# Optimization experiments

Hardware: AMD Instinct MI355X
Metric: run time of the kernel (lower is better)

The kernel has to match this reference:

```python
import jax, jax.numpy as jnp
import numpy as np

F = 128          # feature_size
C = 300          # n_content_dims
V = 100001       # n_nodes + 1 (embedding rows)
N0, N1, N2 = 409600, 40960, 4096   # NodeFlow layer sizes (fanout ~10)
E0, E1 = 409600, 40960             # edges in block0 (L0->L1) and block1 (L1->L2)


def setup_inputs() -> dict:
    key = jax.random.key(0)
    ks = jax.random.split(key, 24)
    std = 1.0 / F
    xav_p = float(np.sqrt(6.0 / (C + F)))   # xavier_uniform for proj Linear(C->F)
    xav_c = float(np.sqrt(6.0 / (2 * F + F)))  # xavier_uniform for conv Linear(2F->F)
    return {
        'nid0': jax.random.randint(ks[0], (N0,), 0, 100000),
        'nid1': jax.random.randint(ks[1], (N1,), 0, 100000),
        'nid2': jax.random.randint(ks[2], (N2,), 0, 100000),
        'content0': jax.random.normal(ks[3], (N0, C), jnp.float32),
        'content1': jax.random.normal(ks[4], (N1, C), jnp.float32),
        'content2': jax.random.normal(ks[5], (N2, C), jnp.float32),
        'block0_src': jax.random.randint(ks[6], (E0,), 0, N0),
        'block0_dst': jax.random.randint(ks[7], (E0,), 0, N1),
        'block1_src': jax.random.randint(ks[8], (E1,), 0, N1),
        'block1_dst': jax.random.randint(ks[9], (E1,), 0, N2),
        'node_emb': jax.random.normal(ks[10], (V, F), jnp.float32) * std,
        'Wp0': jax.random.uniform(ks[11], (F, C), jnp.float32, -xav_p, xav_p),
        'bp0': jnp.zeros((F,), jnp.float32),
        'Wp1': jax.random.uniform(ks[12], (F, C), jnp.float32, -xav_p, xav_p),
        'bp1': jnp.zeros((F,), jnp.float32),
        'Wp2': jax.random.uniform(ks[13], (F, C), jnp.float32, -xav_p, xav_p),
        'bp2': jnp.zeros((F,), jnp.float32),
        'Wc0': jax.random.uniform(ks[14], (F, 2 * F), jnp.float32, -xav_c, xav_c),
        'bc0': jnp.zeros((F,), jnp.float32),
        'Wc1': jax.random.uniform(ks[15], (F, 2 * F), jnp.float32, -xav_c, xav_c),
        'bc1': jnp.zeros((F,), jnp.float32),
    }


def _embed(node_emb, nid, content, Wp, bp):
    # h = node_emb(nid + 1) + LeakyReLU(content @ Wp.T + bp)   (dropout is eval no-op)
    return node_emb[nid + 1] + jax.nn.leaky_relu(content @ Wp.T + bp)


def _conv(h_src, src, dst, h_self, n_dst, W, b):
    # DGL block_compute: copy_src('h')+sum -> h_agg ; copy_src('one')+sum -> w
    msgs = h_src[src]                                    # [E, F] gather
    h_agg = jax.ops.segment_sum(msgs, dst, num_segments=n_dst)
    w = jax.ops.segment_sum(jnp.ones((src.shape[0],), h_src.dtype), dst,
                            num_segments=n_dst)
    h_agg = (h_agg - h_self) / jnp.maximum(w - 1.0, 1.0)[:, None]
    h_new = jax.nn.leaky_relu(jnp.concatenate([h_self, h_agg], axis=1) @ W.T + b)
    nrm = jnp.maximum(jnp.linalg.norm(h_new, axis=1, keepdims=True), 1e-6)
    return h_new / nrm


def reference(nid0, nid1, nid2, content0, content1, content2,
              block0_src, block0_dst, block1_src, block1_dst,
              node_emb, Wp0, bp0, Wp1, bp1, Wp2, bp2,
              Wc0, bc0, Wc1, bc1):
    h0 = _embed(node_emb, nid0, content0, Wp0, bp0)   # [N0, F]
    h1 = _embed(node_emb, nid1, content1, Wp1, bp1)   # [N1, F]
    h2 = _embed(node_emb, nid2, content2, Wp2, bp2)   # [N2, F]
    h1 = _conv(h0, block0_src, block0_dst, h1, N1, Wc0, bc0)
    h2 = _conv(h1, block1_src, block1_dst, h2, N2, Wc1, bc1)
    return h2
```

## Files before the change

### kernel.cpp

```cpp
#include <hip/hip_runtime.h>
#include <hip/hip_bf16.h>
#include <math.h>

#define F 128
#define C 300
#define CKP 320
#define K2F 256
#define N0_ 409600
#define N1_ 40960
#define N2_ 4096
#define E0_ 409600
#define E1_ 40960
#define CAP 64
#define LDA 40

typedef unsigned short u16;
typedef unsigned int u32;
typedef __attribute__((ext_vector_type(8))) short short8;
typedef __attribute__((ext_vector_type(8))) unsigned short u16x8;
typedef __attribute__((ext_vector_type(4))) float f32x4;

__device__ __forceinline__ float lrelu(float x) { return x > 0.f ? x : 0.01f * x; }

__device__ __forceinline__ u16 f2bf(float x) {
  __hip_bfloat16 h = __float2bfloat16(x);
  u16 r; __builtin_memcpy(&r, &h, 2); return r;
}
__device__ __forceinline__ float bf2f(u16 v) {
  union { u32 u; float f; } c; c.u = ((u32)v) << 16; return c.f;
}

#define GLOAD_LDS16(gp, lp) \
  __builtin_amdgcn_global_load_lds( \
      (const __attribute__((address_space(1))) void*)(const void*)(gp), \
      (__attribute__((address_space(3))) void*)(lp), 16, 0, 0)

__global__ __launch_bounds__(256) void zero_kernel(float4* __restrict__ p, int n4) {
  int i = blockIdx.x * 256 + threadIdx.x;
  if (i < n4) p[i] = make_float4(0.f, 0.f, 0.f, 0.f);
}

__global__ __launch_bounds__(256) void convert_all(
    const float* __restrict__ Wp0, const float* __restrict__ Wp1,
    const float* __restrict__ Wp2, const float* __restrict__ Wc0,
    const float* __restrict__ Wc1,
    u16* __restrict__ Wpb0, u16* __restrict__ Wpb1, u16* __restrict__ Wpb2,
    u16* __restrict__ Wcb0, u16* __restrict__ Wcb1)
{
  int i = blockIdx.x * 256 + threadIdx.x;
  const int P = F * CKP, Q = F * K2F;
  const float* W; u16* O; int K, KP, j;
  if      (i < P)         { W = Wp0; O = Wpb0; K = C;   KP = CKP; j = i; }
  else if (i < 2 * P)     { W = Wp1; O = Wpb1; K = C;   KP = CKP; j = i - P; }
  else if (i < 3 * P)     { W = Wp2; O = Wpb2; K = C;   KP = CKP; j = i - 2 * P; }
  else if (i < 3 * P + Q) { W = Wc0; O = Wcb0; K = K2F; KP = K2F; j = i - 3 * P; }
  else if (i < 3 * P + 2 * Q) { W = Wc1; O = Wcb1; K = K2F; KP = K2F; j = i - 3 * P - Q; }
  else return;
  int f = j / KP, k = j - f * KP;
  O[j] = (k < K) ? f2bf(W[(size_t)f * K + k]) : (u16)0;
}

__global__ __launch_bounds__(256) void build_csr(
    const int* __restrict__ b0s, const int* __restrict__ b0d,
    const int* __restrict__ b1s, const int* __restrict__ b1d,
    int* __restrict__ deg0, int* __restrict__ deg1,
    int* __restrict__ csr0, int* __restrict__ csr1)
{
  int e = blockIdx.x * 256 + threadIdx.x;
  if (e < E0_) {
    int d = b0d[e];
    int slot = atomicAdd(&deg0[d], 1);
    if (slot < CAP) csr0[(size_t)d * CAP + slot] = b0s[e];
  } else {
    int e1 = e - E0_;
    if (e1 < E1_) {
      int d = b1d[e1];
      int slot = atomicAdd(&deg1[d], 1);
      if (slot < CAP) csr1[(size_t)d * CAP + slot] = b1s[e1];
    }
  }
}

__global__ __launch_bounds__(256) void embed_mfma(
    const float* __restrict__ content, const u16* __restrict__ Wpb,
    const float* __restrict__ bp, const int* __restrict__ nid,
    const float* __restrict__ emb, u16* __restrict__ out, int ostride,
    const float* __restrict__ zpad)
{
  __shared__ float As[2][128 * 32];
  __shared__ u16  Bs[2][128 * 32];
  const int t = threadIdx.x;
  const int lane = t & 63, w = t >> 6;
  const int row0 = blockIdx.x * 128;

  f32x4 acc[2][8];
#pragma unroll
  for (int fr = 0; fr < 2; ++fr)
#pragma unroll
    for (int fc = 0; fc < 8; ++fc) {
      acc[fr][fc][0] = 0.f; acc[fr][fc][1] = 0.f;
      acc[fr][fc][2] = 0.f; acc[fr][fc][3] = 0.f;
    }

  const int a_rl = lane >> 3, a_u = lane & 7;
  const int b_rl = lane >> 2, b_u = lane & 3;

  auto stage = [&](int buf, int k0) {
#pragma unroll
    for (int i = 0; i < 4; ++i) {
      int r = w * 32 + i * 8 + a_rl;
      int v = a_u ^ (r & 7);
      const float* gp = (k0 == 288 && v >= 3)
          ? (zpad + v * 4)
          : (content + (size_t)(row0 + r) * C + k0 + v * 4);
      GLOAD_LDS16(gp, &As[buf][(w * 32 + i * 8) * 32]);
    }
#pragma unroll
    for (int j = 0; j < 2; ++j) {
      int r = w * 32 + j * 16 + b_rl;
      int v = b_u ^ (r & 3);
      const u16* gp = Wpb + (size_t)r * CKP + k0 + v * 8;
      GLOAD_LDS16(gp, &Bs[buf][(w * 32 + j * 16) * 32]);
    }
  };

  stage(0, 0);
  __syncthreads();

  const int frow = lane & 15, g = lane >> 4;
  const int nt = CKP / 32;
  int cur = 0;
  for (int tstep = 0; tstep < nt; ++tstep) {
    if (tstep + 1 < nt) stage(cur ^ 1, (tstep + 1) * 32);

    const int sw = frow & 7;
    const int u0 = (2 * g) ^ sw, u1 = (2 * g + 1) ^ sw;
    int ra0 = (w * 32 + frow) * 32, ra1 = (w * 32 + 16 + frow) * 32;
    float4 fa00 = *(const float4*)&As[cur][ra0 + u0 * 4];
    float4 fa01 = *(const float4*)&As[cur][ra0 + u1 * 4];
    float4 fa10 = *(const float4*)&As[cur][ra1 + u0 * 4];
    float4 fa11 = *(const float4*)&As[cur][ra1 + u1 * 4];
    u16x8 a0v, a1v;
    a0v[0]=f2bf(fa00.x); a0v[1]=f2bf(fa00.y); a0v[2]=f2bf(fa00.z); a0v[3]=f2bf(fa00.w);
    a0v[4]=f2bf(fa01.x); a0v[5]=f2bf(fa01.y); a0v[6]=f2bf(fa01.z); a0v[7]=f2bf(fa01.w);
    a1v[0]=f2bf(fa10.x); a1v[1]=f2bf(fa10.y); a1v[2]=f2bf(fa10.z); a1v[3]=f2bf(fa10.w);
    a1v[4]=f2bf(fa11.x); a1v[5]=f2bf(fa11.y); a1v[6]=f2bf(fa11.z); a1v[7]=f2bf(fa11.w);
    short8 a0 = *(short8*)&a0v, a1 = *(short8*)&a1v;

    const int bswz = frow & 3;
#pragma unroll
    for (int fc = 0; fc < 8; ++fc) {
      int rb = (fc * 16 + frow) * 32 + (g ^ bswz) * 8;
      short8 b = *(const short8*)&Bs[cur][rb];
      acc[0][fc] = __builtin_amdgcn_mfma_f32_16x16x32_bf16(a0, b, acc[0][fc], 0, 0, 0);
      acc[1][fc] = __builtin_amdgcn_mfma_f32_16x16x32_bf16(a1, b, acc[1][fc], 0, 0, 0);
    }
    __syncthreads();
    cur ^= 1;
  }

  float bpv[8];
#pragma unroll
  for (int fc = 0; fc < 8; ++fc) bpv[fc] = bp[fc * 16 + frow];
#pragma unroll
  for (int fr = 0; fr < 2; ++fr) {
#pragma unroll
    for (int q = 0; q < 4; ++q) {
      int n = row0 + w * 32 + fr * 16 + g * 4 + q;
      int gi = nid[n] + 1;
      const float* erow = emb + (size_t)gi * F;
      u16* orow = out + (size_t)n * ostride;
#pragma unroll
      for (int fc = 0; fc < 8; ++fc) {
        int col = fc * 16 + frow;
        float v = acc[fr][fc][q] + bpv[fc];
        orow[col] = f2bf(erow[col] + lrelu(v));
      }
    }
  }
}

__global__ __launch_bounds__(256) void gather_xa(
    const u16* __restrict__ hsrc, const int* __restrict__ csr,
    const int* __restrict__ deg, u16* __restrict__ xcat)
{
  int d = blockIdx.x * 4 + (threadIdx.x >> 6);
  int lane = threadIdx.x & 63;
  u32 hv = *(const u32*)&xcat[(size_t)d * (2 * F) + lane * 2];
  float h0f = bf2f((u16)(hv & 0xffff)), h1f = bf2f((u16)(hv >> 16));
  int dg = deg[d];
  int n = dg < CAP ? dg : CAP;
  const int* cp = csr + (size_t)d * CAP;
  float s0 = 0.f, s1 = 0.f;
  int j = 0;
  for (; j + 4 <= n; j += 4) {
    int i0 = cp[j], i1 = cp[j + 1], i2 = cp[j + 2], i3 = cp[j + 3];
    u32 v0 = *(const u32*)&hsrc[(size_t)i0 * F + lane * 2];
    u32 v1 = *(const u32*)&hsrc[(size_t)i1 * F + lane * 2];
    u32 v2 = *(const u32*)&hsrc[(size_t)i2 * F + lane * 2];
    u32 v3 = *(const u32*)&hsrc[(size_t)i3 * F + lane * 2];
    s0 += bf2f((u16)(v0 & 0xffff)) + bf2f((u16)(v1 & 0xffff))
        + bf2f((u16)(v2 & 0xffff)) + bf2f((u16)(v3 & 0xffff));
    s1 += bf2f((u16)(v0 >> 16)) + bf2f((u16)(v1 >> 16))
        + bf2f((u16)(v2 >> 16)) + bf2f((u16)(v3 >> 16));
  }
  for (; j < n; ++j) {
    u32 v = *(const u32*)&hsrc[(size_t)cp[j] * F + lane * 2];
    s0 += bf2f((u16)(v & 0xffff));
    s1 += bf2f((u16)(v >> 16));
  }
  float inv = 1.f / fmaxf((float)dg - 1.f, 1.f);
  u16 a0 = f2bf((s0 - h0f) * inv), a1 = f2bf((s1 - h1f) * inv);
  *(u32*)&xcat[(size_t)d * (2 * F) + F + lane * 2] = ((u32)a1 << 16) | a0;
}

template<int F32OUT>
__global__ __launch_bounds__(256) void conv_mfma(
    const u16* __restrict__ xcat, const u16* __restrict__ Wcb,
    const float* __restrict__ bc, u16* __restrict__ outb,
    float* __restrict__ outf)
{
  __shared__ u16 As[128][LDA];
  __shared__ u16 Bs[128][LDA];
  const int t = threadIdx.x;
  const int lane = t & 63, w = t >> 6;
  const int row0 = blockIdx.x * 128;

  f32x4 acc[2][8];
#pragma unroll
  for (int fr = 0; fr < 2; ++fr)
#pragma unroll
    for (int fc = 0; fc < 8; ++fc) {
      acc[fr][fc][0] = 0.f; acc[fr][fc][1] = 0.f;
      acc[fr][fc][2] = 0.f; acc[fr][fc][3] = 0.f;
    }

  for (int k0 = 0; k0 < K2F; k0 += 32) {
    if (k0) __syncthreads();
#pragma unroll
    for (int it = 0; it < 2; ++it) {
      int cc = it * 256 + t;
      int r = cc >> 2, kc = (cc & 3) * 8;
      *(u16x8*)&As[r][kc] = *(const u16x8*)&xcat[(size_t)(row0 + r) * K2F + k0 + kc];
      *(u16x8*)&Bs[r][kc] = *(const u16x8*)&Wcb[(size_t)r * K2F + k0 + kc];
    }
    __syncthreads();

    const int frow = lane & 15;
    const int kc = (lane >> 4) * 8;
    short8 a0 = *(const short8*)&As[w * 32 + frow][kc];
    short8 a1 = *(const short8*)&As[w * 32 + 16 + frow][kc];
#pragma unroll
    for (int fc = 0; fc < 8; ++fc) {
      short8 b = *(const short8*)&Bs[fc * 16 + frow][kc];
      acc[0][fc] = __builtin_amdgcn_mfma_f32_16x16x32_bf16(a0, b, acc[0][fc], 0, 0, 0);
      acc[1][fc] = __builtin_amdgcn_mfma_f32_16x16x32_bf16(a1, b, acc[1][fc], 0, 0, 0);
    }
  }

  float bcv[8];
#pragma unroll
  for (int fc = 0; fc < 8; ++fc) bcv[fc] = bc[fc * 16 + (lane & 15)];
#pragma unroll
  for (int fr = 0; fr < 2; ++fr) {
#pragma unroll
    for (int q = 0; q < 4; ++q) {
      float x[8];
      float ss = 0.f;
#pragma unroll
      for (int fc = 0; fc < 8; ++fc) {
        x[fc] = lrelu(acc[fr][fc][q] + bcv[fc]);
        ss += x[fc] * x[fc];
      }
#pragma unroll
      for (int m = 8; m >= 1; m >>= 1) ss += __shfl_xor(ss, m, 64);
      float nrm = 1.f / fmaxf(sqrtf(ss), 1e-6f);
      int n = row0 + w * 32 + fr * 16 + (lane >> 4) * 4 + q;
#pragma unroll
      for (int fc = 0; fc < 8; ++fc) {
        int col = fc * 16 + (lane & 15);
        if (F32OUT) outf[(size_t)n * F + col] = x[fc] * nrm;
        else        outb[(size_t)n * F + col] = f2bf(x[fc] * nrm);
      }
    }
  }
}

extern "C" void kernel_launch(void* const* d_in, const int* in_sizes, int n_in,
                              void* d_out, int out_size, void* d_ws, size_t ws_size,
                              hipStream_t stream) {
  const int*   nid0     = (const int*)d_in[0];
  const int*   nid1     = (const int*)d_in[1];
  const int*   nid2     = (const int*)d_in[2];
  const float* content0 = (const float*)d_in[3];
  const float* content1 = (const float*)d_in[4];
  const float* content2 = (const float*)d_in[5];
  const int*   b0s      = (const int*)d_in[6];
  const int*   b0d      = (const int*)d_in[7];
  const int*   b1s      = (const int*)d_in[8];
  const int*   b1d      = (const int*)d_in[9];
  const float* emb      = (const float*)d_in[10];
  const float* Wp0      = (const float*)d_in[11];
  const float* bp0      = (const float*)d_in[12];
  const float* Wp1      = (const float*)d_in[13];
  const float* bp1      = (const float*)d_in[14];
  const float* Wp2      = (const float*)d_in[15];
  const float* bp2      = (const float*)d_in[16];
  const float* Wc0      = (const float*)d_in[17];
  const float* bc0      = (const float*)d_in[18];
  const float* Wc1      = (const float*)d_in[19];
  const float* bc1      = (const float*)d_in[20];

  u16* wsu = (u16*)d_ws;
  u16* h0b   = wsu;
  u16* xcat1 = h0b + (size_t)N0_ * F;
  u16* xcat2 = xcat1 + (size_t)N1_ * 2 * F;
  u16* h1nb  = xcat2 + (size_t)N2_ * 2 * F;
  u16* Wpb0  = h1nb + (size_t)N1_ * F;
  u16* Wpb1  = Wpb0 + (size_t)F * CKP;
  u16* Wpb2  = Wpb1 + (size_t)F * CKP;
  u16* Wcb0  = Wpb2 + (size_t)F * CKP;
  u16* Wcb1  = Wcb0 + (size_t)F * K2F;
  float* zpad = (float*)(Wcb1 + (size_t)F * K2F);
  int* deg0  = (int*)(zpad + 64);
  int* deg1  = deg0 + N1_;
  int* csr0  = deg1 + N2_;
  int* csr1  = csr0 + (size_t)N1_ * CAP;

  const int zn4 = (64 + N1_ + N2_) / 4;
  zero_kernel<<<(zn4 + 255) / 256, 256, 0, stream>>>((float4*)zpad, zn4);

  build_csr<<<(E0_ + E1_ + 255) / 256, 256, 0, stream>>>(
      b0s, b0d, b1s, b1d, deg0, deg1, csr0, csr1);

  convert_all<<<(3 * F * CKP + 2 * F * K2F + 255) / 256, 256, 0, stream>>>(
      Wp0, Wp1, Wp2, Wc0, Wc1, Wpb0, Wpb1, Wpb2, Wcb0, Wcb1);

  embed_mfma<<<N0_ / 128, 256, 0, stream>>>(content0, Wpb0, bp0, nid0, emb, h0b, F, zpad);
  embed_mfma<<<N1_ / 128, 256, 0, stream>>>(content1, Wpb1, bp1, nid1, emb, xcat1, 2 * F, zpad);
  embed_mfma<<<N2_ / 128, 256, 0, stream>>>(content2, Wpb2, bp2, nid2, emb, xcat2, 2 * F, zpad);

  gather_xa<<<N1_ / 4, 256, 0, stream>>>(h0b, csr0, deg0, xcat1);
  conv_mfma<0><<<N1_ / 128, 256, 0, stream>>>(xcat1, Wcb0, bc0, h1nb, nullptr);

  gather_xa<<<N2_ / 4, 256, 0, stream>>>(h1nb, csr1, deg1, xcat2);
  conv_mfma<1><<<N2_ / 128, 256, 0, stream>>>(xcat2, Wcb1, bc1, nullptr, (float*)d_out);
}
```

Before: 332.0 us.

## Merge embed launches, keep whole weight in LDS, stream content directly to registers

The three embed launches are fused into one grid that picks its layer's pointers from the block index. The entire bf16 projection weight (10 K-tiles) is loaded into shared memory once per block. The content tile is no longer staged through LDS; each lane loads its A fragments straight from global memory into registers with two-deep software prefetch. The zero-pad buffer goes away and the tail is masked by column index instead. This removes the per-step barriers and double-buffered LDS traffic. In exchange, register pressure rises and the direct global loads are only partly coalesced, since the 300-float row stride is not 16-byte aligned for float4 loads.

```diff
diff --git a/kernel.cpp b/kernel.cpp
--- a/kernel.cpp
+++ b/kernel.cpp
@@ -5,6 +5,7 @@
 #define F 128
 #define C 300
 #define CKP 320
+#define NKT 10
 #define K2F 256
 #define N0_ 409600
 #define N1_ 40960
@@ -81,17 +82,49 @@
   }
 }
 
-__global__ __launch_bounds__(256) void embed_mfma(
-    const float* __restrict__ content, const u16* __restrict__ Wpb,
-    const float* __restrict__ bp, const int* __restrict__ nid,
-    const float* __restrict__ emb, u16* __restrict__ out, int ostride,
-    const float* __restrict__ zpad)
-{
-  __shared__ float As[2][128 * 32];
-  __shared__ u16  Bs[2][128 * 32];
-  const int t = threadIdx.x;
-  const int lane = t & 63, w = t >> 6;
-  const int row0 = blockIdx.x * 128;
+struct Afrag { float4 x00, x01, x10, x11; };
+
+__global__ __launch_bounds__(256, 2) void embed_all(
+    const float* __restrict__ content0, const float* __restrict__ content1,
+    const float* __restrict__ content2,
+    const u16* __restrict__ Wpb0, const u16* __restrict__ Wpb1,
+    const u16* __restrict__ Wpb2,
+    const float* __restrict__ bp0, const float* __restrict__ bp1,
+    const float* __restrict__ bp2,
+    const int* __restrict__ nid0, const int* __restrict__ nid1,
+    const int* __restrict__ nid2,
+    const float* __restrict__ emb,
+    u16* __restrict__ out0, u16* __restrict__ out1, u16* __restrict__ out2)
+{
+  __shared__ u16 Bs[NKT * 128 * 32];
+  const int t = threadIdx.x, lane = t & 63, w = t >> 6;
+  const int b = blockIdx.x;
+
+  const float* content; const u16* Wpb; const float* bp; const int* nid;
+  u16* out; int ostride, row0;
+  if (b < N0_ / 128) {
+    content = content0; Wpb = Wpb0; bp = bp0; nid = nid0;
+    out = out0; ostride = F; row0 = b * 128;
+  } else if (b < N0_ / 128 + N1_ / 128) {
+    content = content1; Wpb = Wpb1; bp = bp1; nid = nid1;
+    out = out1; ostride = 2 * F; row0 = (b - N0_ / 128) * 128;
+  } else {
+    content = content2; Wpb = Wpb2; bp = bp2; nid = nid2;
+    out = out2; ostride = 2 * F; row0 = (b - N0_ / 128 - N1_ / 128) * 128;
+  }
+
+  {
+    const int j_in = lane >> 2, u_in = lane & 3;
+#pragma unroll
+    for (int cc = 0; cc < 20; ++cc) {
+      int c = w * 20 + cc;
+      int kt = c >> 3, j0 = (c & 7) * 16;
+      int j = j0 + j_in;
+      int u = u_in ^ (j & 3);
+      const u16* gp = Wpb + (size_t)j * CKP + kt * 32 + u * 8;
+      GLOAD_LDS16(gp, &Bs[(size_t)(kt * 128 + j0) * 32]);
+    }
+  }
 
   f32x4 acc[2][8];
 #pragma unroll
@@ -102,62 +135,61 @@
       acc[fr][fc][2] = 0.f; acc[fr][fc][3] = 0.f;
     }
 
-  const int a_rl = lane >> 3, a_u = lane & 7;
-  const int b_rl = lane >> 2, b_u = lane & 3;
-
-  auto stage = [&](int buf, int k0) {
-#pragma unroll
-    for (int i = 0; i < 4; ++i) {
-      int r = w * 32 + i * 8 + a_rl;
-      int v = a_u ^ (r & 7);
-      const float* gp = (k0 == 288 && v >= 3)
-          ? (zpad + v * 4)
-          : (content + (size_t)(row0 + r) * C + k0 + v * 4);
-      GLOAD_LDS16(gp, &As[buf][(w * 32 + i * 8) * 32]);
-    }
-#pragma unroll
-    for (int j = 0; j < 2; ++j) {
-      int r = w * 32 + j * 16 + b_rl;
-      int v = b_u ^ (r & 3);
-      const u16* gp = Wpb + (size_t)r * CKP + k0 + v * 8;
-      GLOAD_LDS16(gp, &Bs[buf][(w * 32 + j * 16) * 32]);
-    }
+  const int frow = lane & 15, g = lane >> 4;
+  const float* c0p = content + (size_t)(row0 + w * 32 + frow) * C;
+  const float* c1p = c0p + (size_t)16 * C;
+
+  auto loadA = [&](int kt) -> Afrag {
+    Afrag r;
+    int col = kt * 32 + g * 8;
+    if (kt < NKT - 1) {
+      r.x00 = *(const float4*)(c0p + col); r.x01 = *(const float4*)(c0p + col + 4);
+      r.x10 = *(const float4*)(c1p + col); r.x11 = *(const float4*)(c1p + col + 4);
+    } else {
+      float v0[8], v1[8];
+#pragma unroll
+      for (int i = 0; i < 8; ++i) {
+        int cc = col + i;
+        v0[i] = (cc < C) ? c0p[cc] : 0.f;
+        v1[i] = (cc < C) ? c1p[cc] : 0.f;
+      }
+      r.x00 = make_float4(v0[0], v0[1], v0[2], v0[3]);
+      r.x01 = make_float4(v0[4], v0[5], v0[6], v0[7]);
+      r.x10 = make_float4(v1[0], v1[1], v1[2], v1[3]);
+      r.x11 = make_float4(v1[4], v1[5], v1[6], v1[7]);
+    }
+    return r;
   };
 
-  stage(0, 0);
+  const int bsw = (g ^ (frow & 3)) * 8;
+  auto compute = [&](const Afrag& a, int kt) {
+    u16x8 a0v, a1v;
+    a0v[0]=f2bf(a.x00.x); a0v[1]=f2bf(a.x00.y); a0v[2]=f2bf(a.x00.z); a0v[3]=f2bf(a.x00.w);
+    a0v[4]=f2bf(a.x01.x); a0v[5]=f2bf(a.x01.y); a0v[6]=f2bf(a.x01.z); a0v[7]=f2bf(a.x01.w);
+    a1v[0]=f2bf(a.x10.x); a1v[1]=f2bf(a.x10.y); a1v[2]=f2bf(a.x10.z); a1v[3]=f2bf(a.x10.w);
+    a1v[4]=f2bf(a.x11.x); a1v[5]=f2bf(a.x11.y); a1v[6]=f2bf(a.x11.z); a1v[7]=f2bf(a.x11.w);
+    short8 a0 = *(short8*)&a0v, a1 = *(short8*)&a1v;
+#pragma unroll
+    for (int fc = 0; fc < 8; ++fc) {
+      short8 bfr = *(const short8*)&Bs[(size_t)(kt * 128 + fc * 16 + frow) * 32 + bsw];
+      acc[0][fc] = __builtin_amdgcn_mfma_f32_16x16x32_bf16(a0, bfr, acc[0][fc], 0, 0, 0);
+      acc[1][fc] = __builtin_amdgcn_mfma_f32_16x16x32_bf16(a1, bfr, acc[1][fc], 0, 0, 0);
+    }
+  };
+
+  Afrag A0 = loadA(0);
+  Afrag A1 = loadA(1);
   __syncthreads();
-
-  const int frow = lane & 15, g = lane >> 4;
-  const int nt = CKP / 32;
-  int cur = 0;
-  for (int tstep = 0; tstep < nt; ++tstep) {
-    if (tstep + 1 < nt) stage(cur ^ 1, (tstep + 1) * 32);
-
-    const int sw = frow & 7;
-    const int u0 = (2 * g) ^ sw, u1 = (2 * g + 1) ^ sw;
-    int ra0 = (w * 32 + frow) * 32, ra1 = (w * 32 + 16 + frow) * 32;
-    float4 fa00 = *(const float4*)&As[cur][ra0 + u0 * 4];
-    float4 fa01 = *(const float4*)&As[cur][ra0 + u1 * 4];
-    float4 fa10 = *(const float4*)&As[cur][ra1 + u0 * 4];
-    float4 fa11 = *(const float4*)&As[cur][ra1 + u1 * 4];
-    u16x8 a0v, a1v;
-    a0v[0]=f2bf(fa00.x); a0v[1]=f2bf(fa00.y); a0v[2]=f2bf(fa00.z); a0v[3]=f2bf(fa00.w);
-    a0v[4]=f2bf(fa01.x); a0v[5]=f2bf(fa01.y); a0v[6]=f2bf(fa01.z); a0v[7]=f2bf(fa01.w);
-    a1v[0]=f2bf(fa10.x); a1v[1]=f2bf(fa10.y); a1v[2]=f2bf(fa10.z); a1v[3]=f2bf(fa10.w);
-    a1v[4]=f2bf(fa11.x); a1v[5]=f2bf(fa11.y); a1v[6]=f2bf(fa11.z); a1v[7]=f2bf(fa11.w);
-    short8 a0 = *(short8*)&a0v, a1 = *(short8*)&a1v;
-
-    const int bswz = frow & 3;
-#pragma unroll
-    for (int fc = 0; fc < 8; ++fc) {
-      int rb = (fc * 16 + frow) * 32 + (g ^ bswz) * 8;
-      short8 b = *(const short8*)&Bs[cur][rb];
-      acc[0][fc] = __builtin_amdgcn_mfma_f32_16x16x32_bf16(a0, b, acc[0][fc], 0, 0, 0);
-      acc[1][fc] = __builtin_amdgcn_mfma_f32_16x16x32_bf16(a1, b, acc[1][fc], 0, 0, 0);
-    }
-    __syncthreads();
-    cur ^= 1;
-  }
+  Afrag A2 = loadA(2); compute(A0, 0);
+  Afrag A3 = loadA(3); compute(A1, 1);
+  A0 = loadA(4);       compute(A2, 2);
+  A1 = loadA(5);       compute(A3, 3);
+  A2 = loadA(6);       compute(A0, 4);
+  A3 = loadA(7);       compute(A1, 5);
+  A0 = loadA(8);       compute(A2, 6);
+  A1 = loadA(9);       compute(A3, 7);
+  compute(A0, 8);
+  compute(A1, 9);
 
   float bpv[8];
 #pragma unroll
@@ -321,14 +353,13 @@
   u16* Wpb2  = Wpb1 + (size_t)F * CKP;
   u16* Wcb0  = Wpb2 + (size_t)F * CKP;
   u16* Wcb1  = Wcb0 + (size_t)F * K2F;
-  float* zpad = (float*)(Wcb1 + (size_t)F * K2F);
-  int* deg0  = (int*)(zpad + 64);
+  int* deg0  = (int*)(Wcb1 + (size_t)F * K2F);
   int* deg1  = deg0 + N1_;
   int* csr0  = deg1 + N2_;
   int* csr1  = csr0 + (size_t)N1_ * CAP;
 
-  const int zn4 = (64 + N1_ + N2_) / 4;
-  zero_kernel<<<(zn4 + 255) / 256, 256, 0, stream>>>((float4*)zpad, zn4);
+  const int zn4 = (N1_ + N2_) / 4;
+  zero_kernel<<<(zn4 + 255) / 256, 256, 0, stream>>>((float4*)deg0, zn4);
 
   build_csr<<<(E0_ + E1_ + 255) / 256, 256, 0, stream>>>(
       b0s, b0d, b1s, b1d, deg0, deg1, csr0, csr1);
@@ -336,9 +367,9 @@
   convert_all<<<(3 * F * CKP + 2 * F * K2F + 255) / 256, 256, 0, stream>>>(
       Wp0, Wp1, Wp2, Wc0, Wc1, Wpb0, Wpb1, Wpb2, Wcb0, Wcb1);
 
-  embed_mfma<<<N0_ / 128, 256, 0, stream>>>(content0, Wpb0, bp0, nid0, emb, h0b, F, zpad);
-  embed_mfma<<<N1_ / 128, 256, 0, stream>>>(content1, Wpb1, bp1, nid1, emb, xcat1, 2 * F, zpad);
-  embed_mfma<<<N2_ / 128, 256, 0, stream>>>(content2, Wpb2, bp2, nid2, emb, xcat2, 2 * F, zpad);
+  embed_all<<<(N0_ + N1_ + N2_) / 128, 256, 0, stream>>>(
+      content0, content1, content2, Wpb0, Wpb1, Wpb2,
+      bp0, bp1, bp2, nid0, nid1, nid2, emb, h0b, xcat1, xcat2);
 
   gather_xa<<<N1_ / 4, 256, 0, stream>>>(h0b, csr0, deg0, xcat1);
   conv_mfma<0><<<N1_ / 128, 256, 0, stream>>>(xcat1, Wcb0, bc0, h1nb, nullptr);
```

After: 321.6 us. 1.03x faster.
